# Kernel tuning notes

Hardware: AMD Instinct MI355X
Metric: run time of the kernel (lower is better)

## Reference

```python
import jax, jax.numpy as jnp
import numpy as np

TOP_K = 2
NUM_EXPERTS = 64
SEQ, BS, HS = 2048, 4, 4096
TOKENS = SEQ * BS  # tokens_per_batch
TOL = 1e-4
EPS = 1e-8


def sinkhorn(temp_cost):
    # temp_cost: (T, E) float32 logits. Mirrors SinkhornRouter.sinkhorn exactly.
    cost = jnp.exp(temp_cost)
    n0, n1 = cost.shape
    # initial d0 (overwritten inside loop in torch too, kept for fidelity of carry dtype/shape)
    d0 = (TOKENS / NUM_EXPERTS) * jnp.sum(jnp.exp(2.0 * temp_cost), axis=1)
    d1 = jnp.ones((n1,), dtype=cost.dtype)
    err0 = jnp.asarray(1e9, dtype=cost.dtype)

    def cond(carry):
        _, _, err = carry
        return err > TOL

    def body(carry):
        d0, d1, _ = carry  # d1 here plays the role of d1_old
        d0_new = (1.0 / n0) / (jnp.sum(d1 * cost, axis=1) + EPS)          # (T,)
        d1_new = (1.0 / n1) / (jnp.sum(d0_new[:, None] * cost, axis=0) + EPS)  # (E,)
        err = jnp.mean(jnp.abs(d1 - d1_new))
        return (d0_new, d1_new, err)

    d0, d1, _ = jax.lax.while_loop(cond, body, (d0, d1, err0))
    return d1 * cost * d0[:, None]


def setup_inputs() -> dict:
    key = jax.random.key(0)
    kx, kw = jax.random.split(key)
    x = jax.random.normal(kx, (SEQ, BS, HS), dtype=jnp.float32)
    W = jax.random.normal(kw, (NUM_EXPERTS, HS), dtype=jnp.float32) * 0.02
    return {"x": x, "W": W}


def reference(x, W):
    # router logits: (T, E)
    logits = jnp.reshape(x, (-1, x.shape[-1])) @ W.T
    # Sinkhorn normalization is done in fp32 under no_grad in torch -> stop_gradient
    norm_logits = sinkhorn(jax.lax.stop_gradient(logits).astype(jnp.float32))
    _, indices = jax.lax.top_k(norm_logits, TOP_K)  # (T, top_k) int32
    # top_k > 1 -> softmax activation (fp32, cast back)
    probs = jax.nn.softmax(logits.astype(jnp.float32), axis=-1).astype(logits.dtype)
    scores = jnp.take_along_axis(probs, indices, axis=1)  # (T, top_k)
    return scores, indices
```

## Files before the change

### kernel.cpp

```cpp
#include <hip/hip_runtime.h>
#include <hip/hip_cooperative_groups.h>
#include <math.h>

namespace cg = cooperative_groups;

namespace {
constexpr int kTokens = 8192;
constexpr int kHS = 4096;
constexpr float kTol = 1e-4f;
constexpr float kEps = 1e-8f;
constexpr int kMaxIters = 1000;
constexpr int kSinkBlocks = 32;
constexpr int kSplit = 2;
constexpr size_t kGdataFloats = 2 * 64 * 64 * 2;
constexpr size_t kPartOff = kGdataFloats;
constexpr size_t kPartFloats = (size_t)kTokens * kSplit * 64;
constexpr size_t kWhiOff = kPartOff + kPartFloats;
constexpr size_t kWFragFloats = (size_t)(kHS / 32) * 4 * 64 * 4;
constexpr size_t kWloOff = kWhiOff + kWFragFloats;
constexpr size_t kWsNeedFloats = kWloOff + kWFragFloats;
constexpr size_t kWtpFloats = (size_t)(kHS / 4) * 64 * 4;
}

__device__ __forceinline__ float wave_sum(float v) {
#pragma unroll
  for (int o = 32; o; o >>= 1) v += __shfl_xor(v, o, 64);
  return v;
}

typedef __attribute__((ext_vector_type(8))) short bf16x8;
typedef __attribute__((ext_vector_type(4))) float f32x4;

__device__ __forceinline__ unsigned short f2bf(float x) {
  unsigned u = __builtin_bit_cast(unsigned, x);
  u += 0x7fffu + ((u >> 16) & 1u);
  return (unsigned short)(u >> 16);
}

__device__ __forceinline__ void split8r(const float4 a, const float4 b,
                                        bf16x8& hi, bf16x8& lo) {
  const float v[8] = {a.x, a.y, a.z, a.w, b.x, b.y, b.z, b.w};
#pragma unroll
  for (int j = 0; j < 8; ++j) {
    const unsigned short h = f2bf(v[j]);
    const float hf = __builtin_bit_cast(float, (unsigned)h << 16);
    hi[j] = (short)h;
    lo[j] = (short)f2bf(v[j] - hf);
  }
}

__device__ __forceinline__ void split8(const float* p, bf16x8& hi, bf16x8& lo) {
  split8r(*(const float4*)p, *(const float4*)(p + 4), hi, lo);
}

__global__ void __launch_bounds__(256)
k_wsplit(const float* __restrict__ W, bf16x8* __restrict__ whi,
         bf16x8* __restrict__ wlo) {
  const int idx = blockIdx.x * 256 + threadIdx.x;
  const int lane = idx & 63;
  const int n = (idx >> 6) & 3;
  const int kk = idx >> 8;
  const int e = 16 * n + (lane & 15);
  const int k = kk * 32 + ((lane >> 4) << 3);
  bf16x8 hi, lo;
  split8(W + (size_t)e * kHS + k, hi, lo);
  whi[idx] = hi;
  wlo[idx] = lo;
}

__device__ __forceinline__ void ldB(const bf16x8* __restrict__ bhp,
                                    const bf16x8* __restrict__ blp, int ks,
                                    bf16x8 (&bh)[4], bf16x8 (&bl)[4]) {
#pragma unroll
  for (int n = 0; n < 4; ++n) {
    bh[n] = bhp[(ks * 4 + n) * 64];
    bl[n] = blp[(ks * 4 + n) * 64];
  }
}

__device__ __forceinline__ void ldX(const float* __restrict__ xp, int ks,
                                    float4 (&x)[2][2]) {
#pragma unroll
  for (int m = 0; m < 2; ++m) {
    x[m][0] = *(const float4*)(xp + (size_t)(16 * m) * kHS + ks * 32);
    x[m][1] = *(const float4*)(xp + (size_t)(16 * m) * kHS + ks * 32 + 4);
  }
}

__device__ __forceinline__ void mstep(const float4 (&x)[2][2],
                                      const bf16x8 (&bh)[4],
                                      const bf16x8 (&bl)[4],
                                      f32x4 (&acc)[2][4]) {
#pragma unroll
  for (int m = 0; m < 2; ++m) {
    bf16x8 ah, al;
    split8r(x[m][0], x[m][1], ah, al);
#pragma unroll
    for (int n = 0; n < 4; ++n) {
      acc[m][n] =
          __builtin_amdgcn_mfma_f32_16x16x32_bf16(ah, bh[n], acc[m][n], 0, 0, 0);
      acc[m][n] =
          __builtin_amdgcn_mfma_f32_16x16x32_bf16(al, bh[n], acc[m][n], 0, 0, 0);
      acc[m][n] =
          __builtin_amdgcn_mfma_f32_16x16x32_bf16(ah, bl[n], acc[m][n], 0, 0, 0);
    }
  }
}

__global__ void __launch_bounds__(256, 2)
k_logits(const float* __restrict__ X, const bf16x8* __restrict__ whi,
         const bf16x8* __restrict__ wlo, float* __restrict__ part) {
  const int tid = threadIdx.x;
  const int lane = tid & 63;
  const int wid = tid >> 6;
  const int tile = blockIdx.x >> 1;
  const int sig = blockIdx.x & 1;
  const int t0 = tile * 32;
  const int r = lane & 15;
  const int g = lane >> 4;
  const int kk0 = sig * 64 + wid * 16;

  const float* xp = X + (size_t)(t0 + r) * kHS + kk0 * 32 + g * 8;
  const bf16x8* bhp = whi + (size_t)kk0 * 4 * 64 + lane;
  const bf16x8* blp = wlo + (size_t)kk0 * 4 * 64 + lane;

  f32x4 acc[2][4];
#pragma unroll
  for (int m = 0; m < 2; ++m)
#pragma unroll
    for (int n = 0; n < 4; ++n) acc[m][n] = (f32x4){0.f, 0.f, 0.f, 0.f};

  bf16x8 bhA[4], blA[4], bhB[4], blB[4];
  float4 xA[2][2], xB[2][2];
  ldB(bhp, blp, 0, bhA, blA);
  ldX(xp, 0, xA);

#pragma unroll
  for (int kp = 0; kp < 8; ++kp) {
    const int ks = 2 * kp;
    if (ks + 1 < 16) {
      ldB(bhp, blp, ks + 1, bhB, blB);
      ldX(xp, ks + 1, xB);
    }
    mstep(xA, bhA, blA, acc);
    if (ks + 2 < 16) {
      ldB(bhp, blp, ks + 2, bhA, blA);
      ldX(xp, ks + 2, xA);
    }
    mstep(xB, bhB, blB, acc);
  }

  __shared__ __align__(16) float red[4][32][68];
#pragma unroll
  for (int m = 0; m < 2; ++m)
#pragma unroll
    for (int n = 0; n < 4; ++n)
#pragma unroll
      for (int q = 0; q < 4; ++q)
        red[wid][m * 16 + g * 4 + q][n * 16 + r] = acc[m][n][q];
  __syncthreads();

#pragma unroll
  for (int rep = 0; rep < 2; ++rep) {
    const int idx = rep * 256 + tid;
    const int t = idx >> 4;
    const int e4 = (idx & 15) * 4;
    float4 s = *(const float4*)&red[0][t][e4];
#pragma unroll
    for (int w = 1; w < 4; ++w) {
      const float4 p = *(const float4*)&red[w][t][e4];
      s.x += p.x; s.y += p.y; s.z += p.z; s.w += p.w;
    }
    *(float4*)(part + ((size_t)(tile * 2 + sig) * 32 + t) * 64 + e4) = s;
  }
}

__global__ void __launch_bounds__(1024, 1)
k_sinkhorn(const float* __restrict__ part, float* __restrict__ out,
           unsigned long long* __restrict__ gdata) {
  const int tid = threadIdx.x;
  const int lane = tid & 63;
  const int wid = __builtin_amdgcn_readfirstlane(tid >> 6);
  const int blk = blockIdx.x;
  __shared__ float lds[1024];

  const int t0 = blk * 256 + wid * 16;
  float lg[16], cst[16];
#pragma unroll
  for (int t = 0; t < 16; ++t) {
    const int row = t0 + t;
    const float* pb =
        part + ((size_t)(row >> 5) * 2 * 32 + (row & 31)) * 64 + lane;
    const float a = pb[0] + pb[2048];
    lg[t] = a;
    cst[t] = expf(a);
  }

  float d1 = 1.0f;
  float d0v[16];
  for (int it = 0; it < kMaxIters; ++it) {
    float p = 0.0f;
#pragma unroll
    for (int t = 0; t < 16; ++t) {
      const float s = wave_sum(d1 * cst[t]);
      const float d0t = (1.0f / 8192.0f) / (s + kEps);
      d0v[t] = d0t;
      p = fmaf(d0t, cst[t], p);
    }
    __syncthreads();
    lds[wid * 64 + lane] = p;
    __syncthreads();
    const unsigned want = (unsigned)(it + 1);
    const int buf = it & 1;
    if (wid == 0) {
      float bp = 0.0f;
#pragma unroll
      for (int w = 0; w < 16; ++w) bp += lds[w * 64 + lane];
      const unsigned long long pk =
          ((unsigned long long)want << 32) |
          (unsigned long long)__builtin_bit_cast(unsigned, bp);
      __hip_atomic_store(&gdata[((size_t)buf * 64 + blk) * 64 + lane], pk,
                         __ATOMIC_RELAXED, __HIP_MEMORY_SCOPE_AGENT);
    }
    __syncthreads();
    float s2 = 0.0f;
#pragma unroll
    for (int i = 0; i < 2; ++i) {
      const size_t gi = ((size_t)buf * 64 + wid * 2 + i) * 64 + lane;
      unsigned long long v;
      while (((v = __hip_atomic_load(&gdata[gi], __ATOMIC_RELAXED,
                                     __HIP_MEMORY_SCOPE_AGENT)) >>
              32) != want) {
        __builtin_amdgcn_s_sleep(1);
      }
      s2 += __builtin_bit_cast(float, (unsigned)(v & 0xffffffffu));
    }
    lds[wid * 64 + lane] = s2;
    __syncthreads();
    float colsum = 0.0f;
#pragma unroll
    for (int w = 0; w < 16; ++w) colsum += lds[w * 64 + lane];
    const float d1n = (1.0f / 64.0f) / (colsum + kEps);
    const float err = wave_sum(fabsf(d1 - d1n)) * (1.0f / 64.0f);
    d1 = d1n;
    if (err <= kTol) break;
  }

#pragma unroll
  for (int t = 0; t < 16; ++t) {
    const float lgv = lg[t];
    float m = lgv;
#pragma unroll
    for (int o = 32; o; o >>= 1) m = fmaxf(m, __shfl_xor(m, o, 64));
    const float ex = expf(lgv - m);
    const float den = wave_sum(ex);
    const float prob = ex / den;

    const float v = (d1 * cst[t]) * d0v[t];
    float v1 = v;
    int i1 = lane;
#pragma unroll
    for (int o = 32; o; o >>= 1) {
      const float ov = __shfl_xor(v1, o, 64);
      const int oi = __shfl_xor(i1, o, 64);
      if (ov > v1 || (ov == v1 && oi < i1)) { v1 = ov; i1 = oi; }
    }
    float v2 = (lane == i1) ? -INFINITY : v;
    int i2 = lane;
#pragma unroll
    for (int o = 32; o; o >>= 1) {
      const float ov = __shfl_xor(v2, o, 64);
      const int oi = __shfl_xor(i2, o, 64);
      if (ov > v2 || (ov == v2 && oi < i2)) { v2 = ov; i2 = oi; }
    }
    const float p1 = __shfl(prob, i1, 64);
    const float p2 = __shfl(prob, i2, 64);
    if (lane == 0) {
      const int row = t0 + t;
      out[row * 2 + 0] = p1;
      out[row * 2 + 1] = p2;
      out[2 * kTokens + row * 2 + 0] = (float)i1;
      out[2 * kTokens + row * 2 + 1] = (float)i2;
    }
  }
}

__global__ void __launch_bounds__(256, 1)
sinkhorn_router(const float* __restrict__ X, const float* __restrict__ W,
                float* __restrict__ out, float* __restrict__ ws) {
  cg::grid_group grid = cg::this_grid();
  const int tid = threadIdx.x;
  const int lane = tid & 63;
  const int wid = __builtin_amdgcn_readfirstlane(tid >> 6);
  const int blk = blockIdx.x;

  float4* wtp = reinterpret_cast<float4*>(ws);
  float* gpart = ws + kWtpFloats;
  __shared__ float lds[256];

  {
    const int j = blk * 256 + tid;
    const int e = j & 63;
    const int k4 = j >> 6;
    wtp[j] = *reinterpret_cast<const float4*>(W + (size_t)e * kHS + 4 * (size_t)k4);
  }
  grid.sync();

  const int t0 = blk * 32 + wid * 8;
  const float* xb = X + (size_t)t0 * kHS;
  float lg[8];
#pragma unroll
  for (int t = 0; t < 8; ++t) lg[t] = 0.0f;

#pragma unroll 2
  for (int k4 = 0; k4 < kHS / 4; ++k4) {
    const float4 w = wtp[k4 * 64 + lane];
#pragma unroll
    for (int t = 0; t < 8; ++t) {
      const float* xr = xb + (size_t)t * kHS + 4 * (size_t)k4;
      float a = lg[t];
      a = fmaf(xr[0], w.x, a);
      a = fmaf(xr[1], w.y, a);
      a = fmaf(xr[2], w.z, a);
      a = fmaf(xr[3], w.w, a);
      lg[t] = a;
    }
  }

  float cst[8];
#pragma unroll
  for (int t = 0; t < 8; ++t) cst[t] = expf(lg[t]);

  float d1 = 1.0f;
  float d0v[8];
  int buf = 0;
  for (int it = 0; it < kMaxIters; ++it) {
    float p = 0.0f;
#pragma unroll
    for (int t = 0; t < 8; ++t) {
      const float s = wave_sum(d1 * cst[t]);
      const float d0t = (1.0f / 8192.0f) / (s + kEps);
      d0v[t] = d0t;
      p = fmaf(d0t, cst[t], p);
    }
    __syncthreads();
    lds[wid * 64 + lane] = p;
    __syncthreads();
    if (wid == 0) {
      const float bp =
          lds[lane] + lds[64 + lane] + lds[128 + lane] + lds[192 + lane];
      gpart[buf * (256 * 64) + blk * 64 + lane] = bp;
    }
    grid.sync();
    const float* gp = gpart + buf * (256 * 64);
    float s = 0.0f;
#pragma unroll 8
    for (int b = 0; b < 64; ++b) s += gp[(wid * 64 + b) * 64 + lane];
    lds[wid * 64 + lane] = s;
    __syncthreads();
    const float colsum =
        lds[lane] + lds[64 + lane] + lds[128 + lane] + lds[192 + lane];
    const float d1n = (1.0f / 64.0f) / (colsum + kEps);
    const float err = wave_sum(fabsf(d1 - d1n)) * (1.0f / 64.0f);
    d1 = d1n;
    buf ^= 1;
    if (err <= kTol) break;
  }

#pragma unroll
  for (int t = 0; t < 8; ++t) {
    const float lgv = lg[t];
    float m = lgv;
#pragma unroll
    for (int o = 32; o; o >>= 1) m = fmaxf(m, __shfl_xor(m, o, 64));
    const float ex = expf(lgv - m);
    const float den = wave_sum(ex);
    const float prob = ex / den;

    const float v = (d1 * cst[t]) * d0v[t];
    float v1 = v;
    int i1 = lane;
#pragma unroll
    for (int o = 32; o; o >>= 1) {
      const float ov = __shfl_xor(v1, o, 64);
      const int oi = __shfl_xor(i1, o, 64);
      if (ov > v1 || (ov == v1 && oi < i1)) { v1 = ov; i1 = oi; }
    }
    float v2 = (lane == i1) ? -INFINITY : v;
    int i2 = lane;
#pragma unroll
    for (int o = 32; o; o >>= 1) {
      const float ov = __shfl_xor(v2, o, 64);
      const int oi = __shfl_xor(i2, o, 64);
      if (ov > v2 || (ov == v2 && oi < i2)) { v2 = ov; i2 = oi; }
    }
    const float p1 = __shfl(prob, i1, 64);
    const float p2 = __shfl(prob, i2, 64);
    if (lane == 0) {
      const int row = t0 + t;
      out[row * 2 + 0] = p1;
      out[row * 2 + 1] = p2;
      out[2 * kTokens + row * 2 + 0] = (float)i1;
      out[2 * kTokens + row * 2 + 1] = (float)i2;
    }
  }
}

extern "C" void kernel_launch(void* const* d_in, const int* in_sizes, int n_in,
                              void* d_out, int out_size, void* d_ws,
                              size_t ws_size, hipStream_t stream) {
  const float* X = (const float*)d_in[0];
  const float* W = (const float*)d_in[1];
  float* out = (float*)d_out;
  float* ws = (float*)d_ws;

  const size_t need = kWsNeedFloats * sizeof(float);
  if (ws_size < need) {
    void* args[] = {(void*)&X, (void*)&W, (void*)&out, (void*)&ws};
    hipLaunchCooperativeKernel((const void*)sinkhorn_router, dim3(256),
                               dim3(256), args, 0, stream);
    return;
  }

  unsigned long long* gdata = reinterpret_cast<unsigned long long*>(ws);
  float* part = ws + kPartOff;
  bf16x8* whi = reinterpret_cast<bf16x8*>(ws + kWhiOff);
  bf16x8* wlo = reinterpret_cast<bf16x8*>(ws + kWloOff);

  hipMemsetAsync(gdata, 0, kGdataFloats * sizeof(float), stream);
  hipLaunchKernelGGL(k_wsplit, dim3((kHS / 32) * 4 * 64 / 256), dim3(256), 0,
                     stream, W, whi, wlo);
  hipLaunchKernelGGL(k_logits, dim3((kTokens / 32) * kSplit), dim3(256), 0,
                     stream, X, whi, wlo, part);
  hipLaunchKernelGGL(k_sinkhorn, dim3(kSinkBlocks), dim3(1024), 0, stream,
                     part, out, gdata);
}
```

Before: 254.9 us.

## Increase logits K-split to four and use per-block tag flags for Sinkhorn sync

```diff
diff --git a/kernel.cpp b/kernel.cpp
--- a/kernel.cpp
+++ b/kernel.cpp
@@ -11,9 +11,10 @@
 constexpr float kEps = 1e-8f;
 constexpr int kMaxIters = 1000;
 constexpr int kSinkBlocks = 32;
-constexpr int kSplit = 2;
-constexpr size_t kGdataFloats = 2 * 64 * 64 * 2;
-constexpr size_t kPartOff = kGdataFloats;
+constexpr int kSplit = 4;
+constexpr size_t kTagFloats = 128;
+constexpr size_t kGdataFloats = 2 * 32 * 64;
+constexpr size_t kPartOff = kTagFloats + kGdataFloats;
 constexpr size_t kPartFloats = (size_t)kTokens * kSplit * 64;
 constexpr size_t kWhiOff = kPartOff + kPartFloats;
 constexpr size_t kWFragFloats = (size_t)(kHS / 32) * 4 * 64 * 4;
@@ -107,18 +108,18 @@
   }
 }
 
-__global__ void __launch_bounds__(256, 2)
+__global__ void __launch_bounds__(256, 3)
 k_logits(const float* __restrict__ X, const bf16x8* __restrict__ whi,
          const bf16x8* __restrict__ wlo, float* __restrict__ part) {
   const int tid = threadIdx.x;
   const int lane = tid & 63;
   const int wid = tid >> 6;
-  const int tile = blockIdx.x >> 1;
-  const int sig = blockIdx.x & 1;
+  const int tile = blockIdx.x >> 2;
+  const int sig = blockIdx.x & 3;
   const int t0 = tile * 32;
   const int r = lane & 15;
   const int g = lane >> 4;
-  const int kk0 = sig * 64 + wid * 16;
+  const int kk0 = sig * 32 + wid * 8;
 
   const float* xp = X + (size_t)(t0 + r) * kHS + kk0 * 32 + g * 8;
   const bf16x8* bhp = whi + (size_t)kk0 * 4 * 64 + lane;
@@ -136,14 +137,12 @@
   ldX(xp, 0, xA);
 
 #pragma unroll
-  for (int kp = 0; kp < 8; ++kp) {
+  for (int kp = 0; kp < 4; ++kp) {
     const int ks = 2 * kp;
-    if (ks + 1 < 16) {
-      ldB(bhp, blp, ks + 1, bhB, blB);
-      ldX(xp, ks + 1, xB);
-    }
+    ldB(bhp, blp, ks + 1, bhB, blB);
+    ldX(xp, ks + 1, xB);
     mstep(xA, bhA, blA, acc);
-    if (ks + 2 < 16) {
+    if (ks + 2 < 8) {
       ldB(bhp, blp, ks + 2, bhA, blA);
       ldX(xp, ks + 2, xA);
     }
@@ -171,13 +170,13 @@
       const float4 p = *(const float4*)&red[w][t][e4];
       s.x += p.x; s.y += p.y; s.z += p.z; s.w += p.w;
     }
-    *(float4*)(part + ((size_t)(tile * 2 + sig) * 32 + t) * 64 + e4) = s;
+    *(float4*)(part + ((size_t)(tile * 4 + sig) * 32 + t) * 64 + e4) = s;
   }
 }
 
 __global__ void __launch_bounds__(1024, 1)
 k_sinkhorn(const float* __restrict__ part, float* __restrict__ out,
-           unsigned long long* __restrict__ gdata) {
+           unsigned* __restrict__ tags, float* __restrict__ gdata) {
   const int tid = threadIdx.x;
   const int lane = tid & 63;
   const int wid = __builtin_amdgcn_readfirstlane(tid >> 6);
@@ -190,8 +189,8 @@
   for (int t = 0; t < 16; ++t) {
     const int row = t0 + t;
     const float* pb =
-        part + ((size_t)(row >> 5) * 2 * 32 + (row & 31)) * 64 + lane;
-    const float a = pb[0] + pb[2048];
+        part + ((size_t)(row >> 5) * (kSplit * 32) + (row & 31)) * 64 + lane;
+    const float a = pb[0] + pb[2048] + pb[4096] + pb[6144];
     lg[t] = a;
     cst[t] = expf(a);
   }
@@ -216,25 +215,26 @@
       float bp = 0.0f;
 #pragma unroll
       for (int w = 0; w < 16; ++w) bp += lds[w * 64 + lane];
-      const unsigned long long pk =
-          ((unsigned long long)want << 32) |
-          (unsigned long long)__builtin_bit_cast(unsigned, bp);
-      __hip_atomic_store(&gdata[((size_t)buf * 64 + blk) * 64 + lane], pk,
+      __hip_atomic_store(&gdata[((size_t)buf * 32 + blk) * 64 + lane], bp,
                          __ATOMIC_RELAXED, __HIP_MEMORY_SCOPE_AGENT);
+      __threadfence();
+      if (lane == 0)
+        __hip_atomic_store(&tags[buf * 32 + blk], want, __ATOMIC_RELEASE,
+                           __HIP_MEMORY_SCOPE_AGENT);
+      if (lane < 32) {
+        while (__hip_atomic_load(&tags[buf * 32 + lane], __ATOMIC_ACQUIRE,
+                                 __HIP_MEMORY_SCOPE_AGENT) != want) {
+          __builtin_amdgcn_s_sleep(1);
+        }
+      }
     }
     __syncthreads();
     float s2 = 0.0f;
 #pragma unroll
-    for (int i = 0; i < 2; ++i) {
-      const size_t gi = ((size_t)buf * 64 + wid * 2 + i) * 64 + lane;
-      unsigned long long v;
-      while (((v = __hip_atomic_load(&gdata[gi], __ATOMIC_RELAXED,
-                                     __HIP_MEMORY_SCOPE_AGENT)) >>
-              32) != want) {
-        __builtin_amdgcn_s_sleep(1);
-      }
-      s2 += __builtin_bit_cast(float, (unsigned)(v & 0xffffffffu));
-    }
+    for (int i = 0; i < 2; ++i)
+      s2 += __hip_atomic_load(
+          &gdata[((size_t)buf * 32 + wid * 2 + i) * 64 + lane],
+          __ATOMIC_RELAXED, __HIP_MEMORY_SCOPE_AGENT);
     lds[wid * 64 + lane] = s2;
     __syncthreads();
     float colsum = 0.0f;
@@ -422,16 +422,17 @@
     return;
   }
 
-  unsigned long long* gdata = reinterpret_cast<unsigned long long*>(ws);
+  unsigned* tags = reinterpret_cast<unsigned*>(ws);
+  float* gdata = ws + kTagFloats;
   float* part = ws + kPartOff;
   bf16x8* whi = reinterpret_cast<bf16x8*>(ws + kWhiOff);
   bf16x8* wlo = reinterpret_cast<bf16x8*>(ws + kWloOff);
 
-  hipMemsetAsync(gdata, 0, kGdataFloats * sizeof(float), stream);
+  hipMemsetAsync(tags, 0, kTagFloats * sizeof(float), stream);
   hipLaunchKernelGGL(k_wsplit, dim3((kHS / 32) * 4 * 64 / 256), dim3(256), 0,
                      stream, W, whi, wlo);
   hipLaunchKernelGGL(k_logits, dim3((kTokens / 32) * kSplit), dim3(256), 0,
                      stream, X, whi, wlo, part);
   hipLaunchKernelGGL(k_sinkhorn, dim3(kSinkBlocks), dim3(1024), 0, stream,
-                     part, out, gdata);
-}
+                     part, out, tags, gdata);
+}
```

New measurement: 261.0 us. 2.4% more time.
